# Performance work log

Hardware: AMD Instinct MI355X
Metric: run time of the kernel (lower is better)

The kernel has to match this reference:

```python
import jax, jax.numpy as jnp
import numpy as np

B, S, H, I, E, K = 2, 1024, 768, 1536, 8, 2
CAPACITY_FACTOR = 1.5
ROUTING_TEMP = 1.0
LB_WEIGHT = 0.001


def setup_inputs() -> dict:
    key = jax.random.key(0)
    k_x, k_g, k_w1, k_w3, k_w2 = jax.random.split(key, 5)
    std = 0.02
    return {
        "x": jax.random.normal(k_x, (B, S, H), dtype=jnp.float32),
        "w_gate": jax.random.normal(k_g, (H, E), dtype=jnp.float32) * 0.02,
        "w1": jax.random.normal(k_w1, (E, H, I), dtype=jnp.float32) * std,
        "w3": jax.random.normal(k_w3, (E, H, I), dtype=jnp.float32) * std,
        "w2": jax.random.normal(k_w2, (E, I, H), dtype=jnp.float32) * (std / np.sqrt(2 * 12)),
    }


def _moe_forward(x, w_gate, w1, w3, w2):
    Bb, Ss, Hh = x.shape
    T = Bb * Ss
    xf = x.reshape(T, Hh)

    # --- routing ---
    gate_logits = (xf @ w_gate) / ROUTING_TEMP          # [T, E]
    gate_probs = jax.nn.softmax(gate_logits, axis=-1)   # [T, E]
    topk_probs, topk_idx = jax.lax.top_k(gate_probs, K)  # [T, K]
    topk_probs = topk_probs / (topk_probs.sum(-1, keepdims=True) + 1e-8)

    # --- capacity dropping (per-k slot, token order, like the torch loop) ---
    capacity = max(8, int((T * K // E) * CAPACITY_FACTOR))
    onehot = (topk_idx[:, :, None] == jnp.arange(E)[None, None, :])  # [T, K, E] bool
    ranks = jnp.cumsum(onehot.astype(jnp.int32), axis=0)             # position of token in expert queue
    keep = onehot & (ranks <= capacity)                               # [T, K, E]

    # combine weight per (token, expert): sum over k of kept, clamped routing prob
    w_clamped = jnp.clip(topk_probs, 1e-8, 10.0)                      # [T, K]
    combine = jnp.einsum("tk,tke->te", w_clamped, keep.astype(xf.dtype))  # [T, E]

    # --- dense per-expert SwiGLU (reference form of masked dispatch) ---
    g = jnp.einsum("th,ehi->tei", xf, w1)   # [T, E, I]
    u = jnp.einsum("th,ehi->tei", xf, w3)   # [T, E, I]
    h = jax.nn.silu(g) * u                    # [T, E, I]
    y = jnp.einsum("tei,eih->teh", h, w2)   # [T, E, H]
    out = jnp.einsum("te,teh->th", combine, y).reshape(Bb, Ss, Hh)

    # --- load balancing loss ---
    expert_counts = keep.sum(axis=(0, 1)).astype(jnp.float32)         # [E]
    dropped = (onehot.sum() - keep.sum()).astype(jnp.float32)
    expert_usage = jax.lax.stop_gradient(expert_counts) / float(max(T * K, 1))
    gate_importance = gate_probs.mean(axis=0)                          # [E]
    aux = jnp.sum(expert_usage * gate_importance) * E
    aux = aux + jnp.where(dropped > 0, dropped / float(max(T, 1)) * 0.1, 0.0)
    aux = jnp.minimum(aux, 1.0) * LB_WEIGHT
    return out, aux


def reference(x, w_gate, w1, w3, w2):
    return _moe_forward(x, w_gate, w1, w3, w2)
```

## Files before the change

### kernel.cpp

```cpp
#include <hip/hip_runtime.h>
#include <math.h>

#define T_TOK 2048
#define HD 768
#define ID 1536
#define NE 8
#define CAP 768
#define TK 4096
#define RT 12
#define NB1 24
#define KC1 24
#define NB2 12
#define KC2 48

typedef __bf16 bf16_t;
typedef __bf16 bf16x8 __attribute__((ext_vector_type(8)));
typedef __bf16 bf16x4 __attribute__((ext_vector_type(4)));
typedef float floatx4 __attribute__((ext_vector_type(4)));

__device__ __forceinline__ void gld16(const bf16_t* g, bf16_t* l) {
  __builtin_amdgcn_global_load_lds(
      (__attribute__((address_space(1))) void*)(g),
      (__attribute__((address_space(3))) void*)(l),
      16, 0, 0);
}

__global__ void k_prep(const float* __restrict__ x, const float* __restrict__ wg,
                       const float* __restrict__ w1, const float* __restrict__ w3,
                       const float* __restrict__ w2,
                       bf16_t* __restrict__ xbf, bf16_t* __restrict__ w1b,
                       bf16_t* __restrict__ w3b, bf16_t* __restrict__ w2b,
                       int2* __restrict__ idx2, float2* __restrict__ wc2,
                       float* __restrict__ probs8, float* __restrict__ outz) {
  int b = blockIdx.x;
  int tid = threadIdx.x;
  if (b < 512) {
#pragma unroll
    for (int k2 = 0; k2 < 3; ++k2) {
      float4 z = make_float4(0.f, 0.f, 0.f, 0.f);
      *(float4*)(outz + (size_t)b * 3072 + k2 * 1024 + tid * 4) = z;
    }
    int t = b * 4 + (tid >> 6);
    int lane = tid & 63;
    const float* xr = x + (size_t)t * HD;
    int off = lane * 12;
    float4 a = *(const float4*)(xr + off);
    float4 bv = *(const float4*)(xr + off + 4);
    float4 c = *(const float4*)(xr + off + 8);
    float xv[12] = {a.x, a.y, a.z, a.w, bv.x, bv.y, bv.z, bv.w, c.x, c.y, c.z, c.w};
    bf16x4 s0, s1, s2;
#pragma unroll
    for (int j = 0; j < 4; ++j) { s0[j] = (bf16_t)xv[j]; s1[j] = (bf16_t)xv[4 + j]; s2[j] = (bf16_t)xv[8 + j]; }
    bf16_t* xo = xbf + (size_t)t * HD + off;
    *(bf16x4*)xo = s0; *(bf16x4*)(xo + 4) = s1; *(bf16x4*)(xo + 8) = s2;

    float acc[8] = {0, 0, 0, 0, 0, 0, 0, 0};
#pragma unroll
    for (int jj = 0; jj < 12; ++jj) {
      const float4* wr = (const float4*)(wg + (size_t)(off + jj) * 8);
      float4 w0 = wr[0], w1v = wr[1];
      float v = xv[jj];
      acc[0] += v * w0.x; acc[1] += v * w0.y; acc[2] += v * w0.z; acc[3] += v * w0.w;
      acc[4] += v * w1v.x; acc[5] += v * w1v.y; acc[6] += v * w1v.z; acc[7] += v * w1v.w;
    }
#pragma unroll
    for (int e = 0; e < 8; ++e) {
      float v = acc[e];
      for (int s = 1; s < 64; s <<= 1) v += __shfl_xor(v, s, 64);
      acc[e] = v;
    }
    float mx = acc[0];
#pragma unroll
    for (int e = 1; e < 8; ++e) mx = fmaxf(mx, acc[e]);
    float p[8], sum = 0.f;
#pragma unroll
    for (int e = 0; e < 8; ++e) { p[e] = __expf(acc[e] - mx); sum += p[e]; }
#pragma unroll
    for (int e = 0; e < 8; ++e) p[e] /= sum;
    if (lane == 0) {
      float4 P0 = make_float4(p[0], p[1], p[2], p[3]);
      float4 P1 = make_float4(p[4], p[5], p[6], p[7]);
      *(float4*)&probs8[t * 8] = P0;
      *(float4*)&probs8[t * 8 + 4] = P1;
      int e0 = 0;
#pragma unroll
      for (int e = 1; e < 8; ++e) if (p[e] > p[e0]) e0 = e;
      int e1 = (e0 == 0) ? 1 : 0;
#pragma unroll
      for (int e = 0; e < 8; ++e) if (e != e0 && p[e] > p[e1]) e1 = e;
      float denom = p[e0] + p[e1] + 1e-8f;
      float w0c = fminf(fmaxf(p[e0] / denom, 1e-8f), 10.f);
      float w1c = fminf(fmaxf(p[e1] / denom, 1e-8f), 10.f);
      idx2[t] = make_int2(e0, e1);
      wc2[t] = make_float2(w0c, w1c);
    }
  } else {
    int rb = b - 512;
    const float* src; bf16_t* dst; int C; int kc0;
    if (rb < 1152) {
      int m = rb >= 576;
      int r3 = m ? rb - 576 : rb;
      int pan = r3 / 3;
      kc0 = (r3 - pan * 3) * 8;
      int e = pan & 7, nb = pan >> 3;
      src = (m ? w3 : w1) + (size_t)e * HD * ID + nb * 64;
      dst = (m ? w3b : w1b) + (size_t)(e * NB1 + nb) * (KC1 * 2048);
      C = ID;
    } else {
      int q = rb - 1152;
      int pan = q / 6;
      kc0 = (q - pan * 6) * 8;
      int e = pan & 7, nb = pan >> 3;
      src = w2 + (size_t)e * ID * HD + nb * 64;
      dst = w2b + (size_t)(e * NB2 + nb) * (KC2 * 2048);
      C = HD;
    }
    int n = tid >> 2, p4 = tid & 3;
    int c8 = p4 ^ ((n >> 1) & 3);
    const float* sp0 = src + n + (size_t)(kc0 * 32 + c8 * 8) * C;
    bf16_t* dp = dst + (size_t)kc0 * 2048 + tid * 8;
#pragma unroll 2
    for (int t = 0; t < 8; ++t) {
      const float* sp = sp0 + (size_t)t * 32 * C;
      float v[8];
#pragma unroll
      for (int j = 0; j < 8; ++j) v[j] = sp[(size_t)j * C];
      bf16x8 o;
#pragma unroll
      for (int j = 0; j < 8; ++j) o[j] = (bf16_t)v[j];
      *(bf16x8*)(dp + t * 2048) = o;
    }
  }
}

__global__ void k_scan(const int2* __restrict__ idx2, const float2* __restrict__ wc2,
                       const float* __restrict__ probs8,
                       int* __restrict__ tok_of_row, float* __restrict__ wgt_of_row,
                       int2* __restrict__ cnt_start, float* __restrict__ aux_out) {
  __shared__ int2 sIdx[2048];
  __shared__ float2 sWc[2048];
  __shared__ int sTot[16];
  __shared__ int sPos[8];
  __shared__ float sImp[16][8];
  int tid = threadIdx.x;
  sIdx[tid] = idx2[tid]; sIdx[tid + 1024] = idx2[tid + 1024];
  sWc[tid] = wc2[tid];  sWc[tid + 1024] = wc2[tid + 1024];
  const float4* pp = (const float4*)probs8;
  float4 u0 = pp[tid * 4], u1 = pp[tid * 4 + 1], u2 = pp[tid * 4 + 2], u3 = pp[tid * 4 + 3];
  float im[8] = {u0.x + u2.x, u0.y + u2.y, u0.z + u2.z, u0.w + u2.w,
                 u1.x + u3.x, u1.y + u3.y, u1.z + u3.z, u1.w + u3.w};
#pragma unroll
  for (int e = 0; e < 8; ++e) {
    float v = im[e];
    for (int d = 1; d < 64; d <<= 1) v += __shfl_xor(v, d, 64);
    im[e] = v;
  }
  int w = tid >> 6, lane = tid & 63;
  if (lane == 0) {
#pragma unroll
    for (int e = 0; e < 8; ++e) sImp[w][e] = im[e];
  }
  __syncthreads();
  int s = w >> 3, e = w & 7;
  int t0 = lane * 32;
  int cnt = 0;
  for (int j = 0; j < 32; ++j) {
    int2 p = sIdx[t0 + j];
    cnt += ((s ? p.y : p.x) == e) ? 1 : 0;
  }
  int incl = cnt;
  for (int d = 1; d < 64; d <<= 1) {
    int v = __shfl_up(incl, d, 64);
    if (lane >= d) incl += v;
  }
  int excl = incl - cnt;
  if (lane == 63) sTot[w] = incl;
  __syncthreads();
  if (tid == 0) {
    int run = 0; float a = 0.f;
    for (int ee = 0; ee < 8; ++ee) {
      float impv = 0.f;
      for (int ww = 0; ww < 16; ++ww) impv += sImp[ww][ee];
      int k = min(sTot[ee], CAP) + min(sTot[8 + ee], CAP);
      sPos[ee] = run;
      cnt_start[ee] = make_int2(run, k);
      a += ((float)k / (float)TK) * (impv / (float)T_TOK);
      run += k;
    }
    a *= (float)NE;
    int dropped = TK - run;
    if (dropped > 0) a += (float)dropped / (float)T_TOK * 0.1f;
    aux_out[0] = fminf(a, 1.f) * 0.001f;
  }
  __syncthreads();
  int rank = excl;
  for (int j = 0; j < 32; ++j) {
    int t = t0 + j;
    int2 p = sIdx[t];
    int ex = s ? p.y : p.x;
    if (ex == e) {
      rank++;
      if (rank <= CAP) {
        int pos = atomicAdd(&sPos[e], 1);
        tok_of_row[pos] = t;
        float2 wv = sWc[t];
        wgt_of_row[pos] = s ? wv.y : wv.x;
      }
    }
  }
}

__global__ __launch_bounds__(256, 4)
void k_gemm1(const bf16_t* __restrict__ xbf, const bf16_t* __restrict__ w1b,
             const bf16_t* __restrict__ w3b, const int* __restrict__ tok_of_row,
             const int2* __restrict__ cnt_start, bf16_t* __restrict__ h_ws) {
  int e = blockIdx.x & 7;
  int t = blockIdx.x >> 3;
  int nb = t / RT, rt = t - nb * RT;
  int2 cs = cnt_start[e];
  int nrows = cs.y - rt * 128;
  if (nrows <= 0) return;
  if (nrows > 128) nrows = 128;
  int grow0 = cs.x + rt * 128;

  __shared__ __attribute__((aligned(16))) bf16_t Abuf[128 * 32];
  __shared__ __attribute__((aligned(16))) bf16_t B1buf[64 * 32];
  __shared__ __attribute__((aligned(16))) bf16_t B3buf[64 * 32];

  int tid = threadIdx.x;
  int lane = tid & 63, wv = tid >> 6;
  int wm = wv & 1, wn = wv >> 1;
  int lr = lane & 15, q = lane >> 4;
  int rdc = (q ^ ((lane >> 1) & 3)) * 8;
  int srow = lane >> 2;
  int gch = ((lane & 3) ^ ((lane >> 3) & 3)) * 8;

  int ra = wv * 32 + srow;
  int tokA0 = tok_of_row[grow0 + min(ra, nrows - 1)];
  int tokA1 = tok_of_row[grow0 + min(ra + 16, nrows - 1)];
  const bf16_t* gA0 = xbf + (size_t)tokA0 * HD + gch;
  const bf16_t* gA1 = xbf + (size_t)tokA1 * HD + gch;
  const bf16_t* p1 = w1b + (size_t)((e * NB1 + nb) * KC1) * 2048 + tid * 8;
  const bf16_t* p3 = w3b + (size_t)((e * NB1 + nb) * KC1) * 2048 + tid * 8;
  bf16_t* lA0 = &Abuf[(wv * 32) * 32];
  bf16_t* lA1 = &Abuf[(wv * 32 + 16) * 32];
  bf16_t* lB1 = &B1buf[wv * 512];
  bf16_t* lB3 = &B3buf[wv * 512];

  floatx4 accg[4][2] = {};
  floatx4 accu[4][2] = {};

  for (int kk = 0; kk < KC1; ++kk) {
    __syncthreads();
    gld16(gA0, lA0); gld16(gA1, lA1);
    gld16(p1, lB1); gld16(p3, lB3);
    gA0 += 32; gA1 += 32; p1 += 2048; p3 += 2048;
    __syncthreads();
    bf16x8 af[4], b1f[2], b3f[2];
#pragma unroll
    for (int i = 0; i < 4; ++i) af[i] = *(const bf16x8*)&Abuf[(wm * 64 + i * 16 + lr) * 32 + rdc];
#pragma unroll
    for (int i = 0; i < 2; ++i) b1f[i] = *(const bf16x8*)&B1buf[(wn * 32 + i * 16 + lr) * 32 + rdc];
#pragma unroll
    for (int i = 0; i < 2; ++i) b3f[i] = *(const bf16x8*)&B3buf[(wn * 32 + i * 16 + lr) * 32 + rdc];
#pragma unroll
    for (int i = 0; i < 4; ++i)
#pragma unroll
      for (int jj = 0; jj < 2; ++jj) {
        accg[i][jj] = __builtin_amdgcn_mfma_f32_16x16x32_bf16(af[i], b1f[jj], accg[i][jj], 0, 0, 0);
        accu[i][jj] = __builtin_amdgcn_mfma_f32_16x16x32_bf16(af[i], b3f[jj], accu[i][jj], 0, 0, 0);
      }
  }
#pragma unroll
  for (int i = 0; i < 4; ++i)
#pragma unroll
    for (int r = 0; r < 4; ++r) {
      int rl = wm * 64 + i * 16 + q * 4 + r;
      if (rl < nrows) {
        size_t rb = (size_t)(grow0 + rl) * ID + nb * 64 + wn * 32 + lr;
#pragma unroll
        for (int jj = 0; jj < 2; ++jj) {
          float gg = accg[i][jj][r], uu = accu[i][jj][r];
          float sg = gg / (1.f + __expf(-gg));
          h_ws[rb + jj * 16] = (bf16_t)(sg * uu);
        }
      }
    }
}

__global__ __launch_bounds__(256, 4)
void k_gemm2(const bf16_t* __restrict__ h_ws, const bf16_t* __restrict__ w2b,
             const int* __restrict__ tok_of_row, const float* __restrict__ wgt_of_row,
             const int2* __restrict__ cnt_start, float* __restrict__ out) {
  int e = blockIdx.x & 7;
  int t = blockIdx.x >> 3;
  int nb = t / RT, rt = t - nb * RT;
  int2 cs = cnt_start[e];
  int nrows = cs.y - rt * 128;
  if (nrows <= 0) return;
  if (nrows > 128) nrows = 128;
  int grow0 = cs.x + rt * 128;

  __shared__ __attribute__((aligned(16))) bf16_t Abuf[128 * 32];
  __shared__ __attribute__((aligned(16))) bf16_t Bbuf[64 * 32];

  int tid = threadIdx.x;
  int lane = tid & 63, wv = tid >> 6;
  int wm = wv & 1, wn = wv >> 1;
  int lr = lane & 15, q = lane >> 4;
  int rdc = (q ^ ((lane >> 1) & 3)) * 8;
  int srow = lane >> 2;
  int gch = ((lane & 3) ^ ((lane >> 3) & 3)) * 8;

  int ra = wv * 32 + srow;
  const bf16_t* gA0 = h_ws + (size_t)(grow0 + min(ra, nrows - 1)) * ID + gch;
  const bf16_t* gA1 = h_ws + (size_t)(grow0 + min(ra + 16, nrows - 1)) * ID + gch;
  const bf16_t* pB = w2b + (size_t)((e * NB2 + nb) * KC2) * 2048 + tid * 8;
  bf16_t* lA0 = &Abuf[(wv * 32) * 32];
  bf16_t* lA1 = &Abuf[(wv * 32 + 16) * 32];
  bf16_t* lB = &Bbuf[wv * 512];

  floatx4 acc[4][2] = {};

  for (int kk = 0; kk < KC2; ++kk) {
    __syncthreads();
    gld16(gA0, lA0); gld16(gA1, lA1);
    gld16(pB, lB);
    gA0 += 32; gA1 += 32; pB += 2048;
    __syncthreads();
    bf16x8 af[4], bfr[2];
#pragma unroll
    for (int i = 0; i < 4; ++i) af[i] = *(const bf16x8*)&Abuf[(wm * 64 + i * 16 + lr) * 32 + rdc];
#pragma unroll
    for (int i = 0; i < 2; ++i) bfr[i] = *(const bf16x8*)&Bbuf[(wn * 32 + i * 16 + lr) * 32 + rdc];
#pragma unroll
    for (int i = 0; i < 4; ++i)
#pragma unroll
      for (int jj = 0; jj < 2; ++jj)
        acc[i][jj] = __builtin_amdgcn_mfma_f32_16x16x32_bf16(af[i], bfr[jj], acc[i][jj], 0, 0, 0);
  }
#pragma unroll
  for (int i = 0; i < 4; ++i)
#pragma unroll
    for (int r = 0; r < 4; ++r) {
      int rl = wm * 64 + i * 16 + q * 4 + r;
      if (rl < nrows) {
        int grow = grow0 + rl;
        int tok = tok_of_row[grow];
        float wgt = wgt_of_row[grow];
        size_t ob = (size_t)tok * HD + nb * 64 + wn * 32 + lr;
#pragma unroll
        for (int jj = 0; jj < 2; ++jj)
          atomicAdd(&out[ob + jj * 16], wgt * acc[i][jj][r]);
      }
    }
}

extern "C" void kernel_launch(void* const* d_in, const int* in_sizes, int n_in,
                              void* d_out, int out_size, void* d_ws, size_t ws_size,
                              hipStream_t stream) {
  const float* x  = (const float*)d_in[0];
  const float* wg = (const float*)d_in[1];
  const float* w1 = (const float*)d_in[2];
  const float* w3 = (const float*)d_in[3];
  const float* w2 = (const float*)d_in[4];
  float* out = (float*)d_out;

  char* ws = (char*)d_ws;
  bf16_t* xbf  = (bf16_t*)(ws + 0);
  bf16_t* w1b  = (bf16_t*)(ws + 3145728);
  bf16_t* w3b  = (bf16_t*)(ws + 22020096);
  bf16_t* w2b  = (bf16_t*)(ws + 40894464);
  bf16_t* h_ws = (bf16_t*)(ws + 59768832);
  float*  probs8     = (float*)(ws + 72351744);
  int2*   idx2       = (int2*)(ws + 72417280);
  float2* wc2        = (float2*)(ws + 72433664);
  int*    tok_of_row = (int*)(ws + 72450048);
  float*  wgt_of_row = (float*)(ws + 72466432);
  int2*   cnt_start  = (int2*)(ws + 72482816);

  float* aux_out = out + (size_t)T_TOK * HD;

  k_prep<<<2240, 256, 0, stream>>>(x, wg, w1, w3, w2, xbf, w1b, w3b, w2b,
                                   idx2, wc2, probs8, out);
  k_scan<<<1, 1024, 0, stream>>>(idx2, wc2, probs8, tok_of_row, wgt_of_row,
                                 cnt_start, aux_out);
  k_gemm1<<<8 * NB1 * RT, 256, 0, stream>>>(xbf, w1b, w3b, tok_of_row,
                                            cnt_start, h_ws);
  k_gemm2<<<8 * NB2 * RT, 256, 0, stream>>>(h_ws, w2b, tok_of_row, wgt_of_row,
                                            cnt_start, out);
}
```

Before: 262.2 us.

## Fuse routing scan into prep kernel via flag spin-wait and coalesce weight conversion

```diff
diff --git a/kernel.cpp b/kernel.cpp
--- a/kernel.cpp
+++ b/kernel.cpp
@@ -12,6 +12,7 @@
 #define KC1 24
 #define NB2 12
 #define KC2 48
+#define DONE 0x13572468
 
 typedef __bf16 bf16_t;
 typedef __bf16 bf16x8 __attribute__((ext_vector_type(8)));
@@ -31,7 +32,14 @@
                        bf16_t* __restrict__ xbf, bf16_t* __restrict__ w1b,
                        bf16_t* __restrict__ w3b, bf16_t* __restrict__ w2b,
                        int2* __restrict__ idx2, float2* __restrict__ wc2,
-                       float* __restrict__ probs8, float* __restrict__ outz) {
+                       float* __restrict__ probs8, float* __restrict__ outz,
+                       int* __restrict__ tok_of_row, float* __restrict__ wgt_of_row,
+                       int2* __restrict__ cnt_start, float* __restrict__ aux_out,
+                       int* __restrict__ flags) {
+  __shared__ int2 sIdx[2048];
+  __shared__ int sTot[16];
+  __shared__ int sPos[8];
+  __shared__ float sImp[4][8];
   int b = blockIdx.x;
   int tid = threadIdx.x;
   if (b < 512) {
@@ -93,8 +101,10 @@
       float w1c = fminf(fmaxf(p[e1] / denom, 1e-8f), 10.f);
       idx2[t] = make_int2(e0, e1);
       wc2[t] = make_float2(w0c, w1c);
-    }
-  } else {
+      __threadfence();
+      atomicExch(&flags[t], DONE);
+    }
+  } else if (b < 2240) {
     int rb = b - 512;
     const float* src; bf16_t* dst; int C; int kc0;
     if (rb < 1152) {
@@ -115,96 +125,106 @@
       dst = w2b + (size_t)(e * NB2 + nb) * (KC2 * 2048);
       C = HD;
     }
-    int n = tid >> 2, p4 = tid & 3;
-    int c8 = p4 ^ ((n >> 1) & 3);
-    const float* sp0 = src + n + (size_t)(kc0 * 32 + c8 * 8) * C;
-    bf16_t* dp = dst + (size_t)kc0 * 2048 + tid * 8;
-#pragma unroll 2
-    for (int t = 0; t < 8; ++t) {
-      const float* sp = sp0 + (size_t)t * 32 * C;
-      float v[8];
-#pragma unroll
-      for (int j = 0; j < 8; ++j) v[j] = sp[(size_t)j * C];
-      bf16x8 o;
-#pragma unroll
-      for (int j = 0; j < 8; ++j) o[j] = (bf16_t)v[j];
-      *(bf16x8*)(dp + t * 2048) = o;
-    }
-  }
-}
-
-__global__ void k_scan(const int2* __restrict__ idx2, const float2* __restrict__ wc2,
-                       const float* __restrict__ probs8,
-                       int* __restrict__ tok_of_row, float* __restrict__ wgt_of_row,
-                       int2* __restrict__ cnt_start, float* __restrict__ aux_out) {
-  __shared__ int2 sIdx[2048];
-  __shared__ float2 sWc[2048];
-  __shared__ int sTot[16];
-  __shared__ int sPos[8];
-  __shared__ float sImp[16][8];
-  int tid = threadIdx.x;
-  sIdx[tid] = idx2[tid]; sIdx[tid + 1024] = idx2[tid + 1024];
-  sWc[tid] = wc2[tid];  sWc[tid + 1024] = wc2[tid + 1024];
-  const float4* pp = (const float4*)probs8;
-  float4 u0 = pp[tid * 4], u1 = pp[tid * 4 + 1], u2 = pp[tid * 4 + 2], u3 = pp[tid * 4 + 3];
-  float im[8] = {u0.x + u2.x, u0.y + u2.y, u0.z + u2.z, u0.w + u2.w,
-                 u1.x + u3.x, u1.y + u3.y, u1.z + u3.z, u1.w + u3.w};
-#pragma unroll
-  for (int e = 0; e < 8; ++e) {
-    float v = im[e];
-    for (int d = 1; d < 64; d <<= 1) v += __shfl_xor(v, d, 64);
-    im[e] = v;
-  }
-  int w = tid >> 6, lane = tid & 63;
-  if (lane == 0) {
-#pragma unroll
-    for (int e = 0; e < 8; ++e) sImp[w][e] = im[e];
-  }
-  __syncthreads();
-  int s = w >> 3, e = w & 7;
-  int t0 = lane * 32;
-  int cnt = 0;
-  for (int j = 0; j < 32; ++j) {
-    int2 p = sIdx[t0 + j];
-    cnt += ((s ? p.y : p.x) == e) ? 1 : 0;
-  }
-  int incl = cnt;
-  for (int d = 1; d < 64; d <<= 1) {
-    int v = __shfl_up(incl, d, 64);
-    if (lane >= d) incl += v;
-  }
-  int excl = incl - cnt;
-  if (lane == 63) sTot[w] = incl;
-  __syncthreads();
-  if (tid == 0) {
-    int run = 0; float a = 0.f;
-    for (int ee = 0; ee < 8; ++ee) {
-      float impv = 0.f;
-      for (int ww = 0; ww < 16; ++ww) impv += sImp[ww][ee];
-      int k = min(sTot[ee], CAP) + min(sTot[8 + ee], CAP);
-      sPos[ee] = run;
-      cnt_start[ee] = make_int2(run, k);
-      a += ((float)k / (float)TK) * (impv / (float)T_TOK);
-      run += k;
-    }
-    a *= (float)NE;
-    int dropped = TK - run;
-    if (dropped > 0) a += (float)dropped / (float)T_TOK * 0.1f;
-    aux_out[0] = fminf(a, 1.f) * 0.001f;
-  }
-  __syncthreads();
-  int rank = excl;
-  for (int j = 0; j < 32; ++j) {
-    int t = t0 + j;
-    int2 p = sIdx[t];
-    int ex = s ? p.y : p.x;
-    if (ex == e) {
-      rank++;
-      if (rank <= CAP) {
-        int pos = atomicAdd(&sPos[e], 1);
-        tok_of_row[pos] = t;
-        float2 wv = sWc[t];
-        wgt_of_row[pos] = s ? wv.y : wv.x;
+    int wv = tid >> 6, lane = tid & 63;
+    int g = lane >> 4, m = lane & 15;
+#pragma unroll
+    for (int ti = 0; ti < 2; ++ti) {
+      int kc = kc0 + wv + ti * 4;
+      const float* sp = src + (size_t)(kc * 32 + g * 8) * C + 4 * m;
+      float4 v[8];
+#pragma unroll
+      for (int j = 0; j < 8; ++j) v[j] = *(const float4*)(sp + (size_t)j * C);
+      bf16_t* dp = dst + (size_t)kc * 2048;
+#pragma unroll
+      for (int c = 0; c < 4; ++c) {
+        int n = 4 * m + c;
+        int p = g ^ ((n >> 1) & 3);
+        bf16x8 o;
+#pragma unroll
+        for (int j = 0; j < 8; ++j)
+          o[j] = (bf16_t)((c == 0) ? v[j].x : (c == 1) ? v[j].y : (c == 2) ? v[j].z : v[j].w);
+        *(bf16x8*)(dp + n * 32 + p * 8) = o;
+      }
+    }
+  } else {
+    for (int i = tid; i < 2048; i += 256)
+      while (atomicAdd(&flags[i], 0) != DONE) { }
+    __threadfence();
+    __syncthreads();
+    for (int i = tid; i < 2048; i += 256) sIdx[i] = idx2[i];
+    float im[8] = {0, 0, 0, 0, 0, 0, 0, 0};
+    const float4* pp = (const float4*)probs8;
+#pragma unroll
+    for (int tt = 0; tt < 8; ++tt) {
+      float4 u0 = pp[(tid * 8 + tt) * 2], u1 = pp[(tid * 8 + tt) * 2 + 1];
+      im[0] += u0.x; im[1] += u0.y; im[2] += u0.z; im[3] += u0.w;
+      im[4] += u1.x; im[5] += u1.y; im[6] += u1.z; im[7] += u1.w;
+    }
+    int w = tid >> 6, lane = tid & 63;
+#pragma unroll
+    for (int e = 0; e < 8; ++e) {
+      float v = im[e];
+      for (int d = 1; d < 64; d <<= 1) v += __shfl_xor(v, d, 64);
+      im[e] = v;
+    }
+    if (lane == 0) {
+#pragma unroll
+      for (int e = 0; e < 8; ++e) sImp[w][e] = im[e];
+    }
+    __syncthreads();
+    int t0 = lane * 32;
+    int excl[4];
+#pragma unroll
+    for (int i = 0; i < 4; ++i) {
+      int col = w * 4 + i;
+      int s = col >> 3, e = col & 7;
+      int cnt = 0;
+      for (int j = 0; j < 32; ++j) {
+        int2 p = sIdx[t0 + j];
+        cnt += ((s ? p.y : p.x) == e) ? 1 : 0;
+      }
+      int incl = cnt;
+      for (int d = 1; d < 64; d <<= 1) {
+        int v = __shfl_up(incl, d, 64);
+        if (lane >= d) incl += v;
+      }
+      excl[i] = incl - cnt;
+      if (lane == 63) sTot[col] = incl;
+    }
+    __syncthreads();
+    if (tid == 0) {
+      int run = 0; float a = 0.f;
+      for (int ee = 0; ee < 8; ++ee) {
+        float impv = sImp[0][ee] + sImp[1][ee] + sImp[2][ee] + sImp[3][ee];
+        int k = min(sTot[ee], CAP) + min(sTot[8 + ee], CAP);
+        sPos[ee] = run;
+        cnt_start[ee] = make_int2(run, k);
+        a += ((float)k / (float)TK) * (impv / (float)T_TOK);
+        run += k;
+      }
+      a *= (float)NE;
+      int dropped = TK - run;
+      if (dropped > 0) a += (float)dropped / (float)T_TOK * 0.1f;
+      aux_out[0] = fminf(a, 1.f) * 0.001f;
+    }
+    __syncthreads();
+#pragma unroll
+    for (int i = 0; i < 4; ++i) {
+      int col = w * 4 + i;
+      int s = col >> 3, e = col & 7;
+      int rank = excl[i];
+      for (int j = 0; j < 32; ++j) {
+        int t = t0 + j;
+        int2 p = sIdx[t];
+        if ((s ? p.y : p.x) == e) {
+          rank++;
+          if (rank <= CAP) {
+            int pos = atomicAdd(&sPos[e], 1);
+            tok_of_row[pos] = t;
+            float2 wv2 = wc2[t];
+            wgt_of_row[pos] = s ? wv2.y : wv2.x;
+          }
+        }
       }
     }
   }
@@ -378,13 +398,14 @@
   int*    tok_of_row = (int*)(ws + 72450048);
   float*  wgt_of_row = (float*)(ws + 72466432);
   int2*   cnt_start  = (int2*)(ws + 72482816);
+  int*    flags      = (int*)(ws + 72482880);
 
   float* aux_out = out + (size_t)T_TOK * HD;
 
-  k_prep<<<2240, 256, 0, stream>>>(x, wg, w1, w3, w2, xbf, w1b, w3b, w2b,
-                                   idx2, wc2, probs8, out);
-  k_scan<<<1, 1024, 0, stream>>>(idx2, wc2, probs8, tok_of_row, wgt_of_row,
-                                 cnt_start, aux_out);
+  k_prep<<<2241, 256, 0, stream>>>(x, wg, w1, w3, w2, xbf, w1b, w3b, w2b,
+                                   idx2, wc2, probs8, out,
+                                   tok_of_row, wgt_of_row, cnt_start, aux_out,
+                                   flags);
   k_gemm1<<<8 * NB1 * RT, 256, 0, stream>>>(xbf, w1b, w3b, tok_of_row,
                                             cnt_start, h_ws);
   k_gemm2<<<8 * NB2 * RT, 256, 0, stream>>>(h_ws, w2b, tok_of_row, wgt_of_row,
```

Result: slower. 357.6 us (+36.4%).
